# Optimization experiments

Hardware: AMD Instinct MI355X
Metric: run time of the kernel (lower is better)

## Reference

```python
import jax, jax.numpy as jnp
import numpy as np

B, T, C, H, D = 2, 2048, 1024, 16, 64

def setup_inputs() -> dict:
    key = jax.random.key(0)
    ks = jax.random.split(key, 5)
    s = 1.0 / np.sqrt(C)
    return {
        "hidden_states": jax.random.normal(ks[0], (B, T, C), jnp.float32),
        "Wq": jax.random.normal(ks[1], (H, C, D), jnp.float32) * s,
        "Wk": jax.random.normal(ks[2], (H, C, D), jnp.float32) * s,
        "Wv": jax.random.normal(ks[3], (H, C, D), jnp.float32) * s,
        "Wo": jax.random.normal(ks[4], (C, C), jnp.float32) * s,
    }

def reference(hidden_states, Wq, Wk, Wv, Wo):
    x = hidden_states  # (B, T, C)
    q = jnp.einsum("btc,hcd->bhtd", x, Wq)
    k = jnp.einsum("btc,hcd->bhtd", x, Wk)
    v = jnp.einsum("btc,hcd->bhtd", x, Wv)
    scale = 1.0 / jnp.sqrt(jnp.asarray(D, x.dtype))
    scores = jnp.einsum("bhtd,bhsd->bhts", q, k) * scale  # (B,H,T,T)
    Tlen = x.shape[1]
    causal = jnp.tril(jnp.ones((Tlen, Tlen), bool))
    scores = jnp.where(causal, scores, jnp.asarray(-jnp.inf, x.dtype))
    probs = jax.nn.softmax(scores, axis=-1)
    heads = jnp.einsum("bhts,bhsd->bhtd", probs, v)  # (B,H,T,D)
    concat = heads.transpose(0, 2, 1, 3).reshape(x.shape[0], Tlen, H * D)  # (B,T,C)
    return jnp.einsum("btc,oc->bto", concat, Wo)  # output projection (dropout=0)
```

## Files before the change

kernel.cpp:

```cpp
#include <hip/hip_runtime.h>
#include <math.h>

#define B_ 2
#define T_ 2048
#define C_ 1024
#define H_ 16
#define D_ 64

typedef short short8 __attribute__((ext_vector_type(8)));
typedef float f32x4 __attribute__((ext_vector_type(4)));

#define LOG2E 1.44269504088896f

__device__ __forceinline__ unsigned short f2bf(float f) {
    unsigned int u = __float_as_uint(f);
    u += 0x7FFFu + ((u >> 16) & 1u);
    return (unsigned short)(u >> 16);
}

#define NCAST 2560

__global__ __launch_bounds__(256) void prep_all(
    const float* __restrict__ x,  const float* __restrict__ Wq,
    const float* __restrict__ Wk, const float* __restrict__ Wv,
    const float* __restrict__ Wo,
    unsigned short* __restrict__ xb,   unsigned short* __restrict__ Wall,
    unsigned short* __restrict__ wob,  int nX, int nW)
{
    const int bid = blockIdx.x;
    const int tid = threadIdx.x;
    if (bid < NCAST) {
        int i = (bid * 256 + tid) * 8;
        const float* s;
        unsigned short* d;
        if (i < nX) { s = x + i; d = xb + i; }
        else {
            int j = i - nX;
            if (j >= nW) return;
            s = Wo + j; d = wob + j;
        }
        float4 a = *(const float4*)s;
        float4 b = *(const float4*)(s + 4);
        ushort4 o0, o1;
        o0.x = f2bf(a.x); o0.y = f2bf(a.y); o0.z = f2bf(a.z); o0.w = f2bf(a.w);
        o1.x = f2bf(b.x); o1.y = f2bf(b.y); o1.z = f2bf(b.z); o1.w = f2bf(b.w);
        *(ushort4*)d = o0;
        *(ushort4*)(d + 4) = o1;
        return;
    }
    __shared__ float t[64][65];
    const int tb = bid - NCAST;
    const int c0 = (tb & 15) * 64;
    const int h  = (tb >> 4) & 15;
    const int z  = tb >> 8;
    const float* W = (z == 0) ? Wq : (z == 1) ? Wk : Wv;
    unsigned short* Wt = Wall + (size_t)z * H_ * D_ * C_;
    const int r = tid >> 4, c4 = (tid & 15) * 4;
    #pragma unroll
    for (int p = 0; p < 4; p++) {
        int cl = r + p * 16;
        float4 v = *(const float4*)&W[((size_t)h * C_ + c0 + cl) * D_ + c4];
        t[cl][c4 + 0] = v.x; t[cl][c4 + 1] = v.y;
        t[cl][c4 + 2] = v.z; t[cl][c4 + 3] = v.w;
    }
    __syncthreads();
    #pragma unroll
    for (int p = 0; p < 4; p++) {
        int d = r + p * 16;
        ushort4 o;
        o.x = f2bf(t[c4 + 0][d]); o.y = f2bf(t[c4 + 1][d]);
        o.z = f2bf(t[c4 + 2][d]); o.w = f2bf(t[c4 + 3][d]);
        *(ushort4*)&Wt[((size_t)h * D_ + d) * C_ + c0 + c4] = o;
    }
}

__global__ __launch_bounds__(256) void qkv_big(
    const unsigned short* __restrict__ X,
    const unsigned short* __restrict__ Wall,
    unsigned short* __restrict__ Qo,
    unsigned short* __restrict__ Ko,
    unsigned short* __restrict__ Vt)
{
    __shared__ unsigned short As[128][72];
    __shared__ unsigned short Bs[128][72];

    const int m0 = blockIdx.x * 128;
    const int n0 = blockIdx.y * 128;
    const int z  = n0 >> 10;
    const int tid = threadIdx.x;
    const int w = tid >> 6, lane = tid & 63, quad = lane >> 4, l16 = lane & 15;
    const int wm = w & 1, wn = w >> 1;
    const int lrow = tid >> 3, lcol = (tid & 7) * 8;

    f32x4 acc[4][4] = {};

    short8 ar[4], br[4];
    #pragma unroll
    for (int p = 0; p < 4; p++) {
        int r = lrow + p * 32;
        ar[p] = *(const short8*)&X[(size_t)(m0 + r) * C_ + lcol];
        br[p] = *(const short8*)&Wall[(size_t)(n0 + r) * C_ + lcol];
    }

    for (int k0 = 0; k0 < C_; k0 += 64) {
        __syncthreads();
        #pragma unroll
        for (int p = 0; p < 4; p++) {
            int r = lrow + p * 32;
            *(short8*)&As[r][lcol] = ar[p];
            *(short8*)&Bs[r][lcol] = br[p];
        }
        __syncthreads();
        if (k0 + 64 < C_) {
            #pragma unroll
            for (int p = 0; p < 4; p++) {
                int r = lrow + p * 32;
                ar[p] = *(const short8*)&X[(size_t)(m0 + r) * C_ + k0 + 64 + lcol];
                br[p] = *(const short8*)&Wall[(size_t)(n0 + r) * C_ + k0 + 64 + lcol];
            }
        }
        #pragma unroll
        for (int ks = 0; ks < 2; ks++) {
            short8 af[4], bf[4];
            #pragma unroll
            for (int i = 0; i < 4; i++)
                af[i] = *(const short8*)&As[wm * 64 + i * 16 + l16][ks * 32 + quad * 8];
            #pragma unroll
            for (int j = 0; j < 4; j++)
                bf[j] = *(const short8*)&Bs[wn * 64 + j * 16 + l16][ks * 32 + quad * 8];
            #pragma unroll
            for (int i = 0; i < 4; i++)
                #pragma unroll
                for (int j = 0; j < 4; j++)
                    acc[i][j] = __builtin_amdgcn_mfma_f32_16x16x32_bf16(af[i], bf[j], acc[i][j], 0, 0, 0);
        }
    }

    if (z == 2) {
        #pragma unroll
        for (int j = 0; j < 4; j++) {
            const int n = n0 + wn * 64 + j * 16 + l16;
            const int h = (n >> 6) & 15, d = n & 63;
            #pragma unroll
            for (int i = 0; i < 4; i++) {
                const int m = m0 + wm * 64 + i * 16 + quad * 4;
                const int b = m >> 11, t = m & (T_ - 1);
                ushort4 pk;
                pk.x = f2bf(acc[i][j][0]);
                pk.y = f2bf(acc[i][j][1]);
                pk.z = f2bf(acc[i][j][2]);
                pk.w = f2bf(acc[i][j][3]);
                *(ushort4*)&Vt[(((size_t)b * H_ + h) * D_ + d) * T_ + t] = pk;
            }
        }
    } else {
        const float scale = (z == 0) ? 0.125f * LOG2E : 1.0f;
        unsigned short* O = (z == 0) ? Qo : Ko;
        #pragma unroll
        for (int j = 0; j < 4; j++) {
            const int n = n0 + wn * 64 + j * 16 + l16;
            const int h = (n >> 6) & 15, d = n & 63;
            #pragma unroll
            for (int i = 0; i < 4; i++)
                #pragma unroll
                for (int r = 0; r < 4; r++) {
                    const int m = m0 + wm * 64 + i * 16 + quad * 4 + r;
                    const int b = m >> 11, t = m & (T_ - 1);
                    O[(((size_t)b * H_ + h) * T_ + t) * D_ + d] = f2bf(acc[i][j][r] * scale);
                }
        }
    }
}

__global__ __launch_bounds__(512, 4) void flash_mfma(
    const unsigned short* __restrict__ Q,
    const unsigned short* __restrict__ K,
    const unsigned short* __restrict__ Vt,
    unsigned short* __restrict__ CC)
{
    __shared__ unsigned short kst[64][72];
    __shared__ unsigned short vts[64][72];
    __shared__ unsigned short ps [2][64][72];
    __shared__ float flb[2][64];

    const int d    = blockIdx.x;
    const int x    = d & 7;
    const int loc  = d >> 3;
    const int half = loc >> 5, li = loc & 31;
    const int hsub = li & 3, pr = li >> 2;
    const int p    = half ? (15 - pr) : pr;
    const int head = x * 4 + hsub;
    const int h = head & 15, b = head >> 4;

    const int tid = threadIdx.x;
    const int w = tid >> 6, lane = tid & 63, quad = lane >> 4, l16 = lane & 15;
    const int wg = w & 3;
    const int g  = w >> 2;
    const int lrow = tid >> 3, lcol = (tid & 7) * 8;
    const size_t hb  = ((size_t)b * H_ + h) * T_;
    const size_t hbD = ((size_t)b * H_ + h) * D_;

    const int qb  = g ? (31 - p) : p;
    const int q0  = qb * 64;
    const int myn = qb + 1;
    const int nkb = 32 - p;

    short8 qf[2];
    #pragma unroll
    for (int ks = 0; ks < 2; ks++)
        qf[ks] = *(const short8*)&Q[(hb + q0 + wg * 16 + l16) * D_ + ks * 32 + quad * 8];

    float l_lane = 0.0f;
    f32x4 o[4] = {};

    short8 kreg, vreg;
    kreg = *(const short8*)&K[(hb + lrow) * D_ + lcol];
    vreg = *(const short8*)&Vt[(hbD + lrow) * T_ + lcol];

    for (int kb = 0; kb < nkb; kb++) {
        __syncthreads();
        *(short8*)&kst[lrow][lcol] = kreg;
        *(short8*)&vts[lrow][lcol] = vreg;
        __syncthreads();
        if (kb + 1 < nkb) {
            const int k0n = (kb + 1) * 64;
            kreg = *(const short8*)&K[(hb + k0n + lrow) * D_ + lcol];
            vreg = *(const short8*)&Vt[(hbD + lrow) * T_ + k0n + lcol];
        }

        if (kb < myn) {
            f32x4 s[4] = {};
            __builtin_amdgcn_s_setprio(1);
            #pragma unroll
            for (int ks = 0; ks < 2; ks++)
                #pragma unroll
                for (int ct = 0; ct < 4; ct++) {
                    short8 kf = *(const short8*)&kst[ct * 16 + l16][ks * 32 + quad * 8];
                    s[ct] = __builtin_amdgcn_mfma_f32_16x16x32_bf16(kf, qf[ks], s[ct], 0, 0, 0);
                }
            __builtin_amdgcn_s_setprio(0);

            if (kb == qb) {
                #pragma unroll
                for (int ct = 0; ct < 4; ct++)
                    #pragma unroll
                    for (int r = 0; r < 4; r++)
                        if (ct * 16 + quad * 4 + r > wg * 16 + l16) s[ct][r] = -INFINITY;
            }

            #pragma unroll
            for (int ct = 0; ct < 4; ct++) {
                float e0 = exp2f(s[ct][0]);
                float e1 = exp2f(s[ct][1]);
                float e2 = exp2f(s[ct][2]);
                float e3 = exp2f(s[ct][3]);
                l_lane += (e0 + e1) + (e2 + e3);
                uint2 pk;
                pk.x = __builtin_amdgcn_perm(
                    __float_as_uint(e1) + 0x8000u, __float_as_uint(e0) + 0x8000u, 0x07060302u);
                pk.y = __builtin_amdgcn_perm(
                    __float_as_uint(e3) + 0x8000u, __float_as_uint(e2) + 0x8000u, 0x07060302u);
                *(uint2*)&ps[g][wg * 16 + l16][ct * 16 + quad * 4] = pk;
            }

            __builtin_amdgcn_s_setprio(1);
            #pragma unroll
            for (int ks = 0; ks < 2; ks++) {
                short8 pa = *(const short8*)&ps[g][wg * 16 + l16][ks * 32 + quad * 8];
                #pragma unroll
                for (int ct = 0; ct < 4; ct++) {
                    short8 vf = *(const short8*)&vts[ct * 16 + l16][ks * 32 + quad * 8];
                    o[ct] = __builtin_amdgcn_mfma_f32_16x16x32_bf16(pa, vf, o[ct], 0, 0, 0);
                }
            }
            __builtin_amdgcn_s_setprio(0);
        }
    }

    l_lane += __shfl_xor(l_lane, 16);
    l_lane += __shfl_xor(l_lane, 32);
    if (lane < 16) flb[g][wg * 16 + lane] = l_lane;
    #pragma unroll
    for (int r = 0; r < 4; r++) {
        const int q = wg * 16 + quad * 4 + r;
        const float invl = 1.0f / flb[g][q];
        const int t = q0 + q;
        #pragma unroll
        for (int ct = 0; ct < 4; ct++)
            CC[((size_t)b * T_ + t) * C_ + h * D_ + ct * 16 + l16] = f2bf(o[ct][r] * invl);
    }
}

__global__ __launch_bounds__(256) void out_big(
    const unsigned short* __restrict__ X,
    const unsigned short* __restrict__ Wob,
    float* __restrict__ out)
{
    __shared__ unsigned short As[128][72];
    __shared__ unsigned short Bs[128][72];

    const int m0 = blockIdx.x * 128;
    const int n0 = blockIdx.y * 128;
    const int tid = threadIdx.x;
    const int w = tid >> 6, lane = tid & 63, quad = lane >> 4, l16 = lane & 15;
    const int wm = w & 1, wn = w >> 1;
    const int lrow = tid >> 3, lcol = (tid & 7) * 8;

    f32x4 acc[4][4] = {};

    short8 ar[4], br[4];
    #pragma unroll
    for (int p = 0; p < 4; p++) {
        int r = lrow + p * 32;
        ar[p] = *(const short8*)&X[(size_t)(m0 + r) * C_ + lcol];
        br[p] = *(const short8*)&Wob[(size_t)(n0 + r) * C_ + lcol];
    }

    for (int k0 = 0; k0 < C_; k0 += 64) {
        __syncthreads();
        #pragma unroll
        for (int p = 0; p < 4; p++) {
            int r = lrow + p * 32;
            *(short8*)&As[r][lcol] = ar[p];
            *(short8*)&Bs[r][lcol] = br[p];
        }
        __syncthreads();
        if (k0 + 64 < C_) {
            #pragma unroll
            for (int p = 0; p < 4; p++) {
                int r = lrow + p * 32;
                ar[p] = *(const short8*)&X[(size_t)(m0 + r) * C_ + k0 + 64 + lcol];
                br[p] = *(const short8*)&Wob[(size_t)(n0 + r) * C_ + k0 + 64 + lcol];
            }
        }
        #pragma unroll
        for (int ks = 0; ks < 2; ks++) {
            short8 af[4], bf[4];
            #pragma unroll
            for (int i = 0; i < 4; i++)
                af[i] = *(const short8*)&As[wm * 64 + i * 16 + l16][ks * 32 + quad * 8];
            #pragma unroll
            for (int j = 0; j < 4; j++)
                bf[j] = *(const short8*)&Bs[wn * 64 + j * 16 + l16][ks * 32 + quad * 8];
            #pragma unroll
            for (int i = 0; i < 4; i++)
                #pragma unroll
                for (int j = 0; j < 4; j++)
                    acc[i][j] = __builtin_amdgcn_mfma_f32_16x16x32_bf16(af[i], bf[j], acc[i][j], 0, 0, 0);
        }
    }

    #pragma unroll
    for (int i = 0; i < 4; i++)
        #pragma unroll
        for (int j = 0; j < 4; j++)
            #pragma unroll
            for (int r = 0; r < 4; r++)
                out[(size_t)(m0 + wm * 64 + i * 16 + quad * 4 + r) * C_ + n0 + wn * 64 + j * 16 + l16] = acc[i][j][r];
}

extern "C" void kernel_launch(void* const* d_in, const int* in_sizes, int n_in,
                              void* d_out, int out_size, void* d_ws, size_t ws_size,
                              hipStream_t stream) {
    const float* x  = (const float*)d_in[0];
    const float* Wq = (const float*)d_in[1];
    const float* Wk = (const float*)d_in[2];
    const float* Wv = (const float*)d_in[3];
    const float* Wo = (const float*)d_in[4];
    float* out = (float*)d_out;

    const size_t nX = (size_t)B_ * T_ * C_;
    const size_t nW = (size_t)H_ * C_ * D_;
    const size_t nQ = (size_t)B_ * H_ * T_ * D_;
    unsigned short* xb   = (unsigned short*)d_ws;
    unsigned short* Wall = xb + nX;
    unsigned short* Wob  = Wall + 3 * nW;
    unsigned short* Qb   = Wob + nW;
    unsigned short* Kb   = Qb + nQ;
    unsigned short* Vtb  = Kb + nQ;
    unsigned short* CCb  = Vtb + nQ;

    prep_all<<<dim3(NCAST + 768), 256, 0, stream>>>(
        x, Wq, Wk, Wv, Wo, xb, Wall, Wob, (int)nX, (int)nW);
    qkv_big<<<dim3(32, 24), 256, 0, stream>>>(xb, Wall, Qb, Kb, Vtb);
    flash_mfma<<<dim3(512), 512, 0, stream>>>(Qb, Kb, Vtb, CCb);
    out_big<<<dim3(32, 8), 256, 0, stream>>>(CCb, Wob, out);
}
```

Baseline: 174.8 us.

## Switch flash attention to 32x32x16 MFMA with register-resident probabilities

Rewrites the attention inner loop to use 32x32x16 bf16 MFMAs. Each wave pair splits the key dimension of a 32-query tile, and the probability matrix is rearranged in registers with v_permlane32_swap instead of making an LDS round trip. Partial outputs and row sums from the two key halves are combined through a new float LDS buffer at the end. This removes the per-block P store/load and halves the MFMA instruction count. In exchange it adds an end-of-kernel reduction and a much larger shared-memory footprint, which may cut occupancy below the launch-bounds target.

```diff
diff --git a/kernel.cpp b/kernel.cpp
--- a/kernel.cpp
+++ b/kernel.cpp
@@ -9,6 +9,7 @@
 
 typedef short short8 __attribute__((ext_vector_type(8)));
 typedef float f32x4 __attribute__((ext_vector_type(4)));
+typedef float f32x16 __attribute__((ext_vector_type(16)));
 
 #define LOG2E 1.44269504088896f
 
@@ -180,22 +181,26 @@
 {
     __shared__ unsigned short kst[64][72];
     __shared__ unsigned short vts[64][72];
-    __shared__ unsigned short ps [2][64][72];
-    __shared__ float flb[2][64];
-
-    const int d    = blockIdx.x;
-    const int x    = d & 7;
-    const int loc  = d >> 3;
+    __shared__ float fob[2][64][68];
+    __shared__ float flb_p[2][64];
+    __shared__ float flb_t[2][64];
+
+    const int dd   = blockIdx.x;
+    const int xs   = dd & 7;
+    const int loc  = dd >> 3;
     const int half = loc >> 5, li = loc & 31;
     const int hsub = li & 3, pr = li >> 2;
     const int p    = half ? (15 - pr) : pr;
-    const int head = x * 4 + hsub;
+    const int head = xs * 4 + hsub;
     const int h = head & 15, b = head >> 4;
 
     const int tid = threadIdx.x;
-    const int w = tid >> 6, lane = tid & 63, quad = lane >> 4, l16 = lane & 15;
+    const int w = tid >> 6, lane = tid & 63;
+    const int l31 = lane & 31, hi = lane >> 5;
     const int wg = w & 3;
     const int g  = w >> 2;
+    const int sw = (wg & 1) * 32;
+    const int qw = (wg >> 1) * 32;
     const int lrow = tid >> 3, lcol = (tid & 7) * 8;
     const size_t hb  = ((size_t)b * H_ + h) * T_;
     const size_t hbD = ((size_t)b * H_ + h) * D_;
@@ -205,13 +210,13 @@
     const int myn = qb + 1;
     const int nkb = 32 - p;
 
-    short8 qf[2];
-    #pragma unroll
-    for (int ks = 0; ks < 2; ks++)
-        qf[ks] = *(const short8*)&Q[(hb + q0 + wg * 16 + l16) * D_ + ks * 32 + quad * 8];
+    short8 qf[4];
+    #pragma unroll
+    for (int k4 = 0; k4 < 4; k4++)
+        qf[k4] = *(const short8*)&Q[(hb + q0 + qw + l31) * D_ + k4 * 16 + hi * 8];
 
     float l_lane = 0.0f;
-    f32x4 o[4] = {};
+    f32x16 o0 = {}, o1 = {};
 
     short8 kreg, vreg;
     kreg = *(const short8*)&K[(hb + lrow) * D_ + lcol];
@@ -229,65 +234,90 @@
         }
 
         if (kb < myn) {
-            f32x4 s[4] = {};
+            f32x16 S = {};
             __builtin_amdgcn_s_setprio(1);
             #pragma unroll
-            for (int ks = 0; ks < 2; ks++)
-                #pragma unroll
-                for (int ct = 0; ct < 4; ct++) {
-                    short8 kf = *(const short8*)&kst[ct * 16 + l16][ks * 32 + quad * 8];
-                    s[ct] = __builtin_amdgcn_mfma_f32_16x16x32_bf16(kf, qf[ks], s[ct], 0, 0, 0);
-                }
+            for (int k4 = 0; k4 < 4; k4++) {
+                short8 kf = *(const short8*)&kst[sw + l31][k4 * 16 + hi * 8];
+                S = __builtin_amdgcn_mfma_f32_32x32x16_bf16(kf, qf[k4], S, 0, 0, 0);
+            }
             __builtin_amdgcn_s_setprio(0);
 
             if (kb == qb) {
                 #pragma unroll
-                for (int ct = 0; ct < 4; ct++)
-                    #pragma unroll
-                    for (int r = 0; r < 4; r++)
-                        if (ct * 16 + quad * 4 + r > wg * 16 + l16) s[ct][r] = -INFINITY;
-            }
-
-            #pragma unroll
-            for (int ct = 0; ct < 4; ct++) {
-                float e0 = exp2f(s[ct][0]);
-                float e1 = exp2f(s[ct][1]);
-                float e2 = exp2f(s[ct][2]);
-                float e3 = exp2f(s[ct][3]);
+                for (int reg = 0; reg < 16; reg++) {
+                    const int srel = (reg & 3) + 4 * hi + 8 * (reg >> 2);
+                    if (sw + srel > qw + l31) S[reg] = -INFINITY;
+                }
+            }
+
+            unsigned Wd[8];
+            #pragma unroll
+            for (int blk = 0; blk < 4; blk++) {
+                float e0 = exp2f(S[4 * blk + 0]);
+                float e1 = exp2f(S[4 * blk + 1]);
+                float e2 = exp2f(S[4 * blk + 2]);
+                float e3 = exp2f(S[4 * blk + 3]);
                 l_lane += (e0 + e1) + (e2 + e3);
-                uint2 pk;
-                pk.x = __builtin_amdgcn_perm(
+                Wd[2 * blk + 0] = __builtin_amdgcn_perm(
                     __float_as_uint(e1) + 0x8000u, __float_as_uint(e0) + 0x8000u, 0x07060302u);
-                pk.y = __builtin_amdgcn_perm(
+                Wd[2 * blk + 1] = __builtin_amdgcn_perm(
                     __float_as_uint(e3) + 0x8000u, __float_as_uint(e2) + 0x8000u, 0x07060302u);
-                *(uint2*)&ps[g][wg * 16 + l16][ct * 16 + quad * 4] = pk;
-            }
+            }
+
+            unsigned a0 = Wd[0], b0 = Wd[2];
+            asm("v_permlane32_swap_b32 %0, %1" : "+v"(a0), "+v"(b0));
+            unsigned a1 = Wd[1], b1 = Wd[3];
+            asm("v_permlane32_swap_b32 %0, %1" : "+v"(a1), "+v"(b1));
+            unsigned c0 = Wd[4], d0 = Wd[6];
+            asm("v_permlane32_swap_b32 %0, %1" : "+v"(c0), "+v"(d0));
+            unsigned c1 = Wd[5], d1 = Wd[7];
+            asm("v_permlane32_swap_b32 %0, %1" : "+v"(c1), "+v"(d1));
+            union { unsigned u[4]; short8 v; } pw0, pw1;
+            pw0.u[0] = a0; pw0.u[1] = a1; pw0.u[2] = b0; pw0.u[3] = b1;
+            pw1.u[0] = c0; pw1.u[1] = c1; pw1.u[2] = d0; pw1.u[3] = d1;
 
             __builtin_amdgcn_s_setprio(1);
-            #pragma unroll
-            for (int ks = 0; ks < 2; ks++) {
-                short8 pa = *(const short8*)&ps[g][wg * 16 + l16][ks * 32 + quad * 8];
-                #pragma unroll
-                for (int ct = 0; ct < 4; ct++) {
-                    short8 vf = *(const short8*)&vts[ct * 16 + l16][ks * 32 + quad * 8];
-                    o[ct] = __builtin_amdgcn_mfma_f32_16x16x32_bf16(pa, vf, o[ct], 0, 0, 0);
-                }
+            {
+                short8 vf;
+                vf = *(const short8*)&vts[l31][sw + hi * 8];
+                o0 = __builtin_amdgcn_mfma_f32_32x32x16_bf16(pw0.v, vf, o0, 0, 0, 0);
+                vf = *(const short8*)&vts[l31][sw + 16 + hi * 8];
+                o0 = __builtin_amdgcn_mfma_f32_32x32x16_bf16(pw1.v, vf, o0, 0, 0, 0);
+                vf = *(const short8*)&vts[32 + l31][sw + hi * 8];
+                o1 = __builtin_amdgcn_mfma_f32_32x32x16_bf16(pw0.v, vf, o1, 0, 0, 0);
+                vf = *(const short8*)&vts[32 + l31][sw + 16 + hi * 8];
+                o1 = __builtin_amdgcn_mfma_f32_32x32x16_bf16(pw1.v, vf, o1, 0, 0, 0);
             }
             __builtin_amdgcn_s_setprio(0);
         }
     }
 
-    l_lane += __shfl_xor(l_lane, 16);
     l_lane += __shfl_xor(l_lane, 32);
-    if (lane < 16) flb[g][wg * 16 + lane] = l_lane;
-    #pragma unroll
-    for (int r = 0; r < 4; r++) {
-        const int q = wg * 16 + quad * 4 + r;
-        const float invl = 1.0f / flb[g][q];
-        const int t = q0 + q;
-        #pragma unroll
-        for (int ct = 0; ct < 4; ct++)
-            CC[((size_t)b * T_ + t) * C_ + h * D_ + ct * 16 + l16] = f2bf(o[ct][r] * invl);
+
+    if (wg & 1) {
+        if (lane < 32) flb_p[g][qw + lane] = l_lane;
+        #pragma unroll
+        for (int reg = 0; reg < 16; reg++) {
+            const int qr = (reg & 3) + 4 * hi + 8 * (reg >> 2);
+            fob[g][qw + qr][l31]      = o0[reg];
+            fob[g][qw + qr][32 + l31] = o1[reg];
+        }
+    }
+    __syncthreads();
+    if (!(wg & 1)) {
+        const float lt = l_lane + flb_p[g][qw + l31];
+        if (lane < 32) flb_t[g][qw + lane] = lt;
+        #pragma unroll
+        for (int reg = 0; reg < 16; reg++) {
+            const int qr = (reg & 3) + 4 * hi + 8 * (reg >> 2);
+            const float invl = 1.0f / flb_t[g][qw + qr];
+            const float v0 = o0[reg] + fob[g][qw + qr][l31];
+            const float v1 = o1[reg] + fob[g][qw + qr][32 + l31];
+            const int t = q0 + qw + qr;
+            CC[((size_t)b * T_ + t) * C_ + h * D_ + l31]      = f2bf(v0 * invl);
+            CC[((size_t)b * T_ + t) * C_ + h * D_ + 32 + l31] = f2bf(v1 * invl);
+        }
     }
 }
 
```

New measurement: 172.4 us, median of 2. Within noise of the previous version (-1.4%).
